# Performance work log

Measured on AMD Instinct MI355X. Metric: run time of the kernel, lower is better.

Reference implementation:

```python
import jax, jax.numpy as jnp
import numpy as np
from jax import lax

B, DIM, DIM_OUT, NH = 8, 512, 512, 8
HD = DIM_OUT // NH          # 64, also the depthwise-conv channel count
SQ, SKV = (1, 1), (2, 2)    # stride_q, stride_kv
PAD = 1                      # kernel 3 -> padding 3//2
SCALE = HD ** -0.5
EPS = 1e-6


def _dw_conv(x, w, stride):
    # x: [N, C, H, W], w: [C, 1, kh, kw]; depthwise conv (groups = C), no bias
    return lax.conv_general_dilated(
        x, w, window_strides=stride, padding=[(PAD, PAD), (PAD, PAD)],
        dimension_numbers=('NCHW', 'OIHW', 'NCHW'),
        feature_group_count=x.shape[1])


def _ln(x, w, b):
    m = jnp.mean(x, -1, keepdims=True)
    v = jnp.var(x, -1, keepdims=True)
    return (x - m) * lax.rsqrt(v + EPS) * w + b


def _pool(t, w, stride, ln_w, ln_b, H, W):
    # t: [B, NH, 1+H*W, HD] with cls token at index 0
    Bn = t.shape[0]
    cls = t[:, :, :1, :]
    body = t[:, :, 1:, :].reshape(Bn * NH, H, W, HD).transpose(0, 3, 1, 2)
    body = _dw_conv(body, w, stride)
    ph, pw = body.shape[2], body.shape[3]
    body = body.reshape(Bn, NH, HD, ph * pw).transpose(0, 1, 3, 2)
    out = jnp.concatenate([cls, body], axis=2)
    return _ln(out, ln_w, ln_b), (ph, pw)


def _rel_bias(r_q4, q_shape, k_shape, rel_pos_h, rel_pos_w):
    # r_q4: [B, NH, q_h*q_w, HD] (cls token stripped)
    q_h, q_w = q_shape
    k_h, k_w = k_shape

    def dist(qs, ks):
        qr, kr = max(ks / qs, 1.0), max(qs / ks, 1.0)
        d = np.arange(qs)[:, None] * qr - np.arange(ks)[None, :] * kr + (ks - 1) * kr
        return d.astype(np.int64)

    Rh = rel_pos_h[dist(q_h, k_h)]  # [q_h, k_h, HD]
    Rw = rel_pos_w[dist(q_w, k_w)]  # [q_w, k_w, HD]
    r_q = r_q4.reshape(r_q4.shape[0], NH, q_h, q_w, HD)
    rel_h = jnp.einsum('byhwc,hkc->byhwk', r_q, Rh)  # [B,NH,q_h,q_w,k_h]
    rel_w = jnp.einsum('byhwc,wkc->byhwk', r_q, Rw)  # [B,NH,q_h,q_w,k_w]
    return rel_h[..., :, None] + rel_w[..., None, :]  # [B,NH,q_h,q_w,k_h,k_w]


def setup_inputs() -> dict:
    key = jax.random.key(0)
    ks = jax.random.split(key, 16)
    H = W = 56
    N = H * W + 1
    rel_dim = 2 * H - 1  # 111
    return {
        'x': jax.random.normal(ks[0], (B, N, DIM), jnp.float32),
        'qkv_w': jax.random.normal(ks[1], (3 * DIM_OUT, DIM), jnp.float32) * DIM ** -0.5,
        'qkv_b': jax.random.normal(ks[2], (3 * DIM_OUT,), jnp.float32) * 0.02,
        'proj_w': jax.random.normal(ks[3], (DIM_OUT, DIM_OUT), jnp.float32) * DIM_OUT ** -0.5,
        'proj_b': jax.random.normal(ks[4], (DIM_OUT,), jnp.float32) * 0.02,
        'pool_q_w': jax.random.normal(ks[5], (HD, 1, 3, 3), jnp.float32) / 3.0,
        'pool_k_w': jax.random.normal(ks[6], (HD, 1, 3, 3), jnp.float32) / 3.0,
        'pool_v_w': jax.random.normal(ks[7], (HD, 1, 3, 3), jnp.float32) / 3.0,
        'lnq_w': 1.0 + 0.1 * jax.random.normal(ks[8], (HD,), jnp.float32),
        'lnq_b': 0.02 * jax.random.normal(ks[9], (HD,), jnp.float32),
        'lnk_w': 1.0 + 0.1 * jax.random.normal(ks[10], (HD,), jnp.float32),
        'lnk_b': 0.02 * jax.random.normal(ks[11], (HD,), jnp.float32),
        'lnv_w': 1.0 + 0.1 * jax.random.normal(ks[12], (HD,), jnp.float32),
        'lnv_b': 0.02 * jax.random.normal(ks[13], (HD,), jnp.float32),
        'rel_pos_h': 0.02 * jax.random.normal(ks[14], (rel_dim, HD), jnp.float32),
        'rel_pos_w': 0.02 * jax.random.normal(ks[15], (rel_dim, HD), jnp.float32),
        'hw_h': 56,
        'hw_w': 56,
    }


def reference(x, qkv_w, qkv_b, proj_w, proj_b, pool_q_w, pool_k_w, pool_v_w,
              lnq_w, lnq_b, lnk_w, lnk_b, lnv_w, lnv_b, rel_pos_h, rel_pos_w,
              hw_h, hw_w):
    Bn, N, _ = x.shape
    qkv = (x @ qkv_w.T + qkv_b).reshape(Bn, N, 3, NH, HD).transpose(2, 0, 3, 1, 4)
    q, k, v = qkv[0], qkv[1], qkv[2]  # each [B, NH, N, HD]
    q, q_shape = _pool(q, pool_q_w, SQ, lnq_w, lnq_b, hw_h, hw_w)
    k, k_shape = _pool(k, pool_k_w, SKV, lnk_w, lnk_b, hw_h, hw_w)
    v, _ = _pool(v, pool_v_w, SKV, lnv_w, lnv_b, hw_h, hw_w)
    attn = (q * SCALE) @ k.swapaxes(-2, -1)  # [B, NH, Nq, Nk]
    q_h, q_w = q_shape
    k_h, k_w = k_shape
    bias = _rel_bias(q[:, :, 1:, :], q_shape, k_shape, rel_pos_h, rel_pos_w)
    blk = attn[:, :, 1:, 1:].reshape(Bn, NH, q_h, q_w, k_h, k_w) + bias
    attn = attn.at[:, :, 1:, 1:].set(blk.reshape(Bn, NH, q_h * q_w, k_h * k_w))
    attn = jax.nn.softmax(attn, axis=-1)
    out = attn @ v                                   # [B, NH, Nq, HD]
    out = out.at[:, :, 1:, :].add(q[:, :, 1:, :])    # residual on non-cls rows
    out = out.transpose(0, 2, 1, 3).reshape(Bn, -1, DIM_OUT)
    return out @ proj_w.T + proj_b
```

## Files before the change

### kernel.cpp

```cpp
#include <hip/hip_runtime.h>
#include <hip/hip_bf16.h>
#include <cstdint>
#include <cstddef>

#define BB 8
#define NHH 8
#define NQ 3137
#define NKV 785
#define HDIM 64
#define AUG 128
#define MROWS (BB*NQ)
#define SCALE 0.125f
#define VTP 832

typedef unsigned short ushort_t;
typedef __attribute__((ext_vector_type(8))) short s16x8;
typedef __attribute__((ext_vector_type(4))) float f32x4;
typedef __attribute__((ext_vector_type(16))) float f32x16;

__device__ __forceinline__ float bf2f(ushort_t u) {
  union { unsigned int i; float f; } v; v.i = ((unsigned int)u) << 16; return v.f;
}
__device__ __forceinline__ ushort_t f2bf(float f) {
  union { float f; unsigned int i; } v; v.f = f;
  unsigned int r = v.i + 0x7fffu + ((v.i >> 16) & 1u);
  return (ushort_t)(r >> 16);
}
__device__ __forceinline__ unsigned int cvt_pk_bf16(float lo, float hi) {
  unsigned int r;
  asm("v_cvt_pk_bf16_f32 %0, %1, %2" : "=v"(r) : "v"(lo), "v"(hi));
  return r;
}
__device__ __forceinline__ s16x8 lds_frag8(const ushort_t* base, int row, int slot) {
  const char* p = (const char*)base + row * 128 + (((slot ^ (row & 7)) & 7) << 4);
  return *(const s16x8*)p;
}
__device__ __forceinline__ s16x8 lds_frag16(const ushort_t* base, int row, int slot) {
  const char* p = (const char*)base + row * 256 + (((slot ^ (row & 15)) & 15) << 4);
  return *(const s16x8*)p;
}

template<int EPI, bool AF32, bool WF32>
__global__ __launch_bounds__(256) void mfma_gemm_bt(
    const void* __restrict__ Ap, const void* __restrict__ Wp,
    const float* __restrict__ bias, void* __restrict__ outp, int M) {
  __shared__ ushort_t As[128][40];
  __shared__ ushort_t Bs[128][40];
  const int tid = threadIdx.x;
  const int l = tid & 63, w = tid >> 6;
  const int wr = w >> 1, wc = w & 1;
  const int lrow = l & 15, lk = l >> 4;
  const int m0 = blockIdx.y * 128, n0 = blockIdx.x * 128;
  const int srow = tid >> 2, sch = tid & 3;
  const int mA0 = m0 + srow      < M ? m0 + srow      : M - 1;
  const int mA1 = m0 + 64 + srow < M ? m0 + 64 + srow : M - 1;
  const size_t ar0 = (size_t)mA0 * 512, ar1 = (size_t)mA1 * 512;
  const size_t br0 = (size_t)(n0 + srow) * 512, br1 = (size_t)(n0 + 64 + srow) * 512;
  const ushort_t* Ab = (const ushort_t*)Ap;
  const float*    Af = (const float*)Ap;
  const ushort_t* Wb = (const ushort_t*)Wp;
  const float*    Wf = (const float*)Wp;
  auto ld8 = [&](const ushort_t* pb, const float* pf, size_t ofs, bool f32) -> uint4 {
    if (!f32) return *(const uint4*)(pb + ofs);
    const float4 v0 = *(const float4*)(pf + ofs);
    const float4 v1 = *(const float4*)(pf + ofs + 4);
    uint4 r;
    r.x = cvt_pk_bf16(v0.x, v0.y); r.y = cvt_pk_bf16(v0.z, v0.w);
    r.z = cvt_pk_bf16(v1.x, v1.y); r.w = cvt_pk_bf16(v1.z, v1.w);
    return r;
  };
  f32x4 acc[4][4];
  #pragma unroll
  for (int i = 0; i < 4; ++i) {
    #pragma unroll
    for (int j = 0; j < 4; ++j) acc[i][j] = (f32x4){0.f, 0.f, 0.f, 0.f};
  }
  for (int k0 = 0; k0 < 512; k0 += 32) {
    const uint4 a0 = ld8(Ab, Af, ar0 + k0 + sch * 8, AF32);
    const uint4 a1 = ld8(Ab, Af, ar1 + k0 + sch * 8, AF32);
    const uint4 b0 = ld8(Wb, Wf, br0 + k0 + sch * 8, WF32);
    const uint4 b1 = ld8(Wb, Wf, br1 + k0 + sch * 8, WF32);
    __syncthreads();
    *(uint4*)(&As[srow][sch * 8])      = a0;
    *(uint4*)(&As[64 + srow][sch * 8]) = a1;
    *(uint4*)(&Bs[srow][sch * 8])      = b0;
    *(uint4*)(&Bs[64 + srow][sch * 8]) = b1;
    __syncthreads();
    s16x8 af[4], bfr[4];
    #pragma unroll
    for (int mi = 0; mi < 4; ++mi)
      af[mi] = *(const s16x8*)(&As[wr * 64 + mi * 16 + lrow][lk * 8]);
    #pragma unroll
    for (int ni = 0; ni < 4; ++ni)
      bfr[ni] = *(const s16x8*)(&Bs[wc * 64 + ni * 16 + lrow][lk * 8]);
    #pragma unroll
    for (int mi = 0; mi < 4; ++mi) {
      #pragma unroll
      for (int ni = 0; ni < 4; ++ni)
        acc[mi][ni] = __builtin_amdgcn_mfma_f32_16x16x32_bf16(
            af[mi], bfr[ni], acc[mi][ni], 0, 0, 0);
    }
  }
  #pragma unroll
  for (int mi = 0; mi < 4; ++mi) {
    #pragma unroll
    for (int r = 0; r < 4; ++r) {
      const int m = m0 + wr * 64 + mi * 16 + 4 * lk + r;
      if (m >= M) continue;
      #pragma unroll
      for (int ni = 0; ni < 4; ++ni) {
        const int n = n0 + wc * 64 + ni * 16 + lrow;
        const float v = acc[mi][ni][r] + bias[n];
        if (EPI == 0) {
          const int which = n >> 9, y = (n >> 6) & 7, c = n & 63;
          const int b_ = m / NQ, tok = m - b_ * NQ;
          ((ushort_t*)outp)[((((size_t)which * BB + b_) * NHH + y) * NQ + tok) * HDIM + c] = f2bf(v);
        } else {
          ((float*)outp)[(size_t)m * 512 + n] = v;
        }
      }
    }
  }
}

template<int MODE>
__global__ __launch_bounds__(256) void pool_ln_kernel(
    const ushort_t* __restrict__ in, ushort_t* __restrict__ out0,
    ushort_t* __restrict__ out1,
    const float* __restrict__ cw, const float* __restrict__ lnw,
    const float* __restrict__ lnb, int stride, int OW, int R) {
  const int tid = threadIdx.x;
  const int c = tid & 63;
  const int rid = blockIdx.x * 4 + (tid >> 6);
  const int by = rid / R;
  const int n = rid - by * R;
  const ushort_t* ibase = in + (size_t)by * NQ * HDIM;
  float val;
  if (n == 0) {
    val = bf2f(ibase[c]);
  } else {
    const int p = n - 1;
    const int ho = p / OW, wo = p - ho * OW;
    float s = 0.f;
    #pragma unroll
    for (int dh = 0; dh < 3; ++dh) {
      const int hh = ho * stride + dh - 1;
      if (hh < 0 || hh >= 56) continue;
      #pragma unroll
      for (int dw = 0; dw < 3; ++dw) {
        const int ww = wo * stride + dw - 1;
        if (ww < 0 || ww >= 56) continue;
        s += cw[c * 9 + dh * 3 + dw] * bf2f(ibase[(size_t)(1 + hh * 56 + ww) * HDIM + c]);
      }
    }
    val = s;
  }
  float sum = val, sq = val * val;
  #pragma unroll
  for (int off = 32; off > 0; off >>= 1) {
    sum += __shfl_xor(sum, off);
    sq  += __shfl_xor(sq,  off);
  }
  const float mean = sum * (1.f / 64.f);
  const float var  = sq * (1.f / 64.f) - mean * mean;
  const float rs = rsqrtf(var + 1e-6f);
  const float lno = (val - mean) * rs * lnw[c] + lnb[c];
  if (MODE == 0) {
    out0[(size_t)rid * HDIM + c] = f2bf(lno);
  } else if (MODE == 1) {
    out0[(size_t)rid * HDIM + c] = f2bf(lno);
    out1[(size_t)rid * AUG + c] = f2bf(lno * SCALE);
    out1[(size_t)rid * AUG + 64 + c] = 0;
  } else {
    out0[(size_t)rid * AUG + c] = f2bf(lno);
    ushort_t aug = 0;
    if (n >= 1) {
      const int p = n - 1;
      const int kh = p / 28, kw = p - 28 * kh;
      if (c < 28) { if (c == kh) aug = 0x3F80; }
      else if (c < 56) { if (c - 28 == kw) aug = 0x3F80; }
    }
    out0[(size_t)rid * AUG + 64 + c] = aug;
  }
}

__global__ __launch_bounds__(256) void transpose_v_kernel(
    const ushort_t* __restrict__ vin, ushort_t* __restrict__ vtout) {
  __shared__ ushort_t T[64][65];
  const int tid = threadIdx.x;
  const int by = blockIdx.y;
  const int n0 = blockIdx.x * 64;
  #pragma unroll
  for (int half = 0; half < 2; ++half) {
    const int idx = tid + half * 256;
    const int r = idx >> 3, s = idx & 7;
    const int n = n0 + r;
    uint4 d = make_uint4(0u, 0u, 0u, 0u);
    if (n < NKV) d = *(const uint4*)(vin + ((size_t)by * NKV + n) * HDIM + s * 8);
    const ushort_t* dp = (const ushort_t*)&d;
    #pragma unroll
    for (int e = 0; e < 8; ++e) T[r][s * 8 + e] = dp[e];
  }
  __syncthreads();
  #pragma unroll
  for (int half = 0; half < 2; ++half) {
    const int idx = tid + half * 256;
    const int c = idx >> 3, g = idx & 7;
    ushort_t pk[8];
    #pragma unroll
    for (int e = 0; e < 8; ++e) pk[e] = T[g * 8 + e][c];
    *(uint4*)(vtout + ((size_t)by * 64 + c) * VTP + n0 + g * 8) = *(const uint4*)pk;
  }
}

__global__ __launch_bounds__(256) void relbias_mfma_kernel(
    const ushort_t* __restrict__ qb, const float* __restrict__ rph,
    const float* __restrict__ rpw, ushort_t* __restrict__ qaug) {
  const int tid = threadIdx.x;
  const int l = tid & 63, w = tid >> 6;
  const int lrow = l & 15, lk = l >> 4;
  const int hw = blockIdx.y;
  const int mode = blockIdx.z;
  const int r0 = blockIdx.x * 256 + w * 64;
  const float* tab = mode ? rpw : rph;
  s16x8 bfr[2][2];
  #pragma unroll
  for (int ni = 0; ni < 2; ++ni) {
    const int kh = ni * 16 + lrow;
    int trow = hw - 2 * kh + 54;
    if (trow < 0) trow = 0;
    const float* tr = tab + (size_t)trow * 64 + lk * 8;
    #pragma unroll
    for (int k0 = 0; k0 < 2; ++k0) {
      const float4 t0 = *(const float4*)(tr + k0 * 32);
      const float4 t1 = *(const float4*)(tr + k0 * 32 + 4);
      s16x8 bb;
      bb[0] = (short)f2bf(t0.x); bb[1] = (short)f2bf(t0.y);
      bb[2] = (short)f2bf(t0.z); bb[3] = (short)f2bf(t0.w);
      bb[4] = (short)f2bf(t1.x); bb[5] = (short)f2bf(t1.y);
      bb[6] = (short)f2bf(t1.z); bb[7] = (short)f2bf(t1.w);
      bfr[ni][k0] = bb;
    }
  }
  s16x8 af[4][2];
  #pragma unroll
  for (int mi = 0; mi < 4; ++mi) {
    const int rA = r0 + mi * 16 + lrow;
    const int by = rA / 56, oth = rA - 56 * by;
    const int tok = mode ? (1 + oth * 56 + hw) : (1 + hw * 56 + oth);
    const ushort_t* qp = qb + ((size_t)by * NQ + tok) * HDIM + lk * 8;
    af[mi][0] = *(const s16x8*)(qp);
    af[mi][1] = *(const s16x8*)(qp + 32);
  }
  f32x4 acc[4][2];
  #pragma unroll
  for (int mi = 0; mi < 4; ++mi) {
    #pragma unroll
    for (int ni = 0; ni < 2; ++ni) acc[mi][ni] = (f32x4){0.f, 0.f, 0.f, 0.f};
  }
  #pragma unroll
  for (int k0 = 0; k0 < 2; ++k0) {
    #pragma unroll
    for (int mi = 0; mi < 4; ++mi) {
      #pragma unroll
      for (int ni = 0; ni < 2; ++ni)
        acc[mi][ni] = __builtin_amdgcn_mfma_f32_16x16x32_bf16(
            af[mi][k0], bfr[ni][k0], acc[mi][ni], 0, 0, 0);
    }
  }
  const int augofs = 64 + mode * 28;
  #pragma unroll
  for (int mi = 0; mi < 4; ++mi) {
    #pragma unroll
    for (int r = 0; r < 4; ++r) {
      const int row = r0 + mi * 16 + 4 * lk + r;
      const int by = row / 56, oth = row - 56 * by;
      const int tok = 1 + (mode ? (oth * 56 + hw) : (hw * 56 + oth));
      ushort_t* orow = qaug + ((size_t)by * NQ + tok) * AUG + augofs;
      #pragma unroll
      for (int ni = 0; ni < 2; ++ni) {
        const int kh = ni * 16 + lrow;
        if (kh < 28) orow[kh] = f2bf(acc[mi][ni][r]);
      }
    }
  }
}

__global__ __launch_bounds__(256) void attn_mfma32_kernel(
    const ushort_t* __restrict__ qaug, const ushort_t* __restrict__ kaug,
    const ushort_t* __restrict__ qb, const ushort_t* __restrict__ vt,
    ushort_t* __restrict__ outp) {
  __shared__ ushort_t Kl[64 * AUG];
  __shared__ ushort_t Vl[64 * 64];
  const int tid = threadIdx.x;
  const int l = tid & 63;
  const int w = tid >> 6;
  const int h = l >> 5, q5 = l & 31;
  const int by = blockIdx.y;
  const int qt0 = blockIdx.x * 128;
  const int qloc = w * 32 + q5;
  const int qglob = qt0 + qloc;
  const int qcl = qglob < NQ ? qglob : NQ - 1;
  const ushort_t* qrow = qaug + ((size_t)by * NQ + qcl) * AUG;
  s16x8 qf[8];
  #pragma unroll
  for (int cb = 0; cb < 8; ++cb)
    qf[cb] = *(const s16x8*)(qrow + cb * 16 + h * 8);
  f32x16 ot0, ot1;
  #pragma unroll
  for (int i = 0; i < 16; ++i) { ot0[i] = 0.f; ot1[i] = 0.f; }
  float mr = -1e30f, lr = 0.f;
  const int krow = tid >> 2, ks4 = (tid & 3) * 4;
  const int vrow = tid >> 3, vslot = tid & 7;
  const ushort_t* kbase = kaug + (size_t)by * NKV * AUG + ks4 * 8;
  const ushort_t* vbase0 = vt + ((size_t)by * 64 + vrow) * VTP + vslot * 8;
  const ushort_t* vbase1 = vt + ((size_t)by * 64 + vrow + 32) * VTP + vslot * 8;
  uint4 kreg[4], vreg[2];
  auto load_tile = [&](int j0) {
    int jK = j0 + krow; if (jK > NKV - 1) jK = NKV - 1;
    const ushort_t* ksrc = kbase + (size_t)jK * AUG;
    kreg[0] = *(const uint4*)(ksrc);
    kreg[1] = *(const uint4*)(ksrc + 8);
    kreg[2] = *(const uint4*)(ksrc + 16);
    kreg[3] = *(const uint4*)(ksrc + 24);
    vreg[0] = *(const uint4*)(vbase0 + j0);
    vreg[1] = *(const uint4*)(vbase1 + j0);
  };
  auto store_tile = [&]() {
    char* kb_ = (char*)Kl + krow * 256;
    const int rm = krow & 15;
    *(uint4*)(kb_ + (((ks4 + 0) ^ rm) << 4)) = kreg[0];
    *(uint4*)(kb_ + (((ks4 + 1) ^ rm) << 4)) = kreg[1];
    *(uint4*)(kb_ + (((ks4 + 2) ^ rm) << 4)) = kreg[2];
    *(uint4*)(kb_ + (((ks4 + 3) ^ rm) << 4)) = kreg[3];
    *(uint4*)((char*)Vl + vrow * 128 + (((vslot ^ (vrow & 7)) & 7) << 4)) = vreg[0];
    *(uint4*)((char*)Vl + (vrow + 32) * 128 + (((vslot ^ ((vrow + 32) & 7)) & 7) << 4)) = vreg[1];
  };
  load_tile(0);
  #pragma unroll 1
  for (int it = 0; it < 13; ++it) {
    __syncthreads();
    store_tile();
    __syncthreads();
    if (it < 12) load_tile((it + 1) * 64);
    f32x16 st0, st1;
    #pragma unroll
    for (int i = 0; i < 16; ++i) { st0[i] = 0.f; st1[i] = 0.f; }
    __builtin_amdgcn_s_setprio(1);
    #pragma unroll
    for (int cb = 0; cb < 8; ++cb) {
      st0 = __builtin_amdgcn_mfma_f32_32x32x16_bf16(
          lds_frag16(Kl, q5, cb * 2 + h), qf[cb], st0, 0, 0, 0);
      st1 = __builtin_amdgcn_mfma_f32_32x32x16_bf16(
          lds_frag16(Kl, 32 + q5, cb * 2 + h), qf[cb], st1, 0, 0, 0);
    }
    __builtin_amdgcn_s_setprio(0);
    if (it == 12) {
      #pragma unroll
      for (int r = 0; r < 16; ++r) {
        const int klocal = (r & 3) + 8 * (r >> 2) + 4 * h;
        if (768 + klocal >= NKV) st0[r] = -1e30f;
        st1[r] = -1e30f;
      }
    }
    float mloc = st0[0];
    #pragma unroll
    for (int r = 1; r < 16; ++r) mloc = fmaxf(mloc, st0[r]);
    #pragma unroll
    for (int r = 0; r < 16; ++r) mloc = fmaxf(mloc, st1[r]);
    mloc = fmaxf(mloc, __shfl_xor(mloc, 32));
    if (!__all(mloc <= mr + 8.f)) {
      const float mn = fmaxf(mr, mloc);
      const float sc = __expf(mr - mn);
      mr = mn;
      lr *= sc;
      #pragma unroll
      for (int i = 0; i < 16; ++i) { ot0[i] *= sc; ot1[i] *= sc; }
    }
    float ps = 0.f;
    #pragma unroll
    for (int r = 0; r < 16; ++r) { st0[r] = __expf(st0[r] - mr); ps += st0[r]; }
    #pragma unroll
    for (int r = 0; r < 16; ++r) { st1[r] = __expf(st1[r] - mr); ps += st1[r]; }
    ps += __shfl_xor(ps, 32);
    lr += ps;
    auto pvstep = [&](const f32x16& pv, int kt) {
      #pragma unroll
      for (int kbk = 0; kbk < 2; ++kbk) {
        const unsigned int pk01 = cvt_pk_bf16(pv[kbk * 8 + 0], pv[kbk * 8 + 1]);
        const unsigned int pk23 = cvt_pk_bf16(pv[kbk * 8 + 2], pv[kbk * 8 + 3]);
        const unsigned int pk45 = cvt_pk_bf16(pv[kbk * 8 + 4], pv[kbk * 8 + 5]);
        const unsigned int pk67 = cvt_pk_bf16(pv[kbk * 8 + 6], pv[kbk * 8 + 7]);
        const unsigned int sA = (unsigned int)__shfl_xor((int)pk01, 32);
        const unsigned int sB = (unsigned int)__shfl_xor((int)pk45, 32);
        const unsigned int sC = (unsigned int)__shfl_xor((int)pk23, 32);
        const unsigned int sD = (unsigned int)__shfl_xor((int)pk67, 32);
        int4 fw;
        fw.x = (int)(h ? sB : pk01);
        fw.y = (int)(h ? sD : pk23);
        fw.z = (int)(h ? pk45 : sA);
        fw.w = (int)(h ? pk67 : sC);
        s16x8 pf;
        __builtin_memcpy(&pf, &fw, 16);
        const int slot = kt * 4 + kbk * 2 + h;
        __builtin_amdgcn_s_setprio(1);
        ot0 = __builtin_amdgcn_mfma_f32_32x32x16_bf16(
            lds_frag8(Vl, q5, slot), pf, ot0, 0, 0, 0);
        ot1 = __builtin_amdgcn_mfma_f32_32x32x16_bf16(
            lds_frag8(Vl, 32 + q5, slot), pf, ot1, 0, 0, 0);
        __builtin_amdgcn_s_setprio(0);
      }
    };
    pvstep(st0, 0);
    pvstep(st1, 1);
  }
  const float inv = 1.f / lr;
  if (qglob < NQ) {
    const int b_ = by >> 3, y_ = by & 7;
    ushort_t* obase = outp + ((size_t)b_ * NQ + qglob) * 512 + (size_t)y_ * 64;
    const ushort_t* rbase = qb + ((size_t)by * NQ + qglob) * HDIM;
    #pragma unroll
    for (int ch = 0; ch < 2; ++ch) {
      #pragma unroll
      for (int rg = 0; rg < 4; ++rg) {
        const int c0 = ch * 32 + 8 * rg + 4 * h;
        float vv[4];
        #pragma unroll
        for (int e = 0; e < 4; ++e)
          vv[e] = (ch ? ot1[rg * 4 + e] : ot0[rg * 4 + e]) * inv;
        if (qglob > 0) {
          #pragma unroll
          for (int e = 0; e < 4; ++e) vv[e] += bf2f(rbase[c0 + e]);
        }
        ushort_t pk[4] = { f2bf(vv[0]), f2bf(vv[1]), f2bf(vv[2]), f2bf(vv[3]) };
        *(uint2*)(obase + c0) = *(const uint2*)pk;
      }
    }
  }
}

extern "C" void kernel_launch(void* const* d_in, const int* in_sizes, int n_in,
                              void* d_out, int out_size, void* d_ws, size_t ws_size,
                              hipStream_t stream) {
  const float* x        = (const float*)d_in[0];
  const float* qkv_w    = (const float*)d_in[1];
  const float* qkv_b    = (const float*)d_in[2];
  const float* proj_w   = (const float*)d_in[3];
  const float* proj_b   = (const float*)d_in[4];
  const float* pool_q_w = (const float*)d_in[5];
  const float* pool_k_w = (const float*)d_in[6];
  const float* pool_v_w = (const float*)d_in[7];
  const float* lnq_w    = (const float*)d_in[8];
  const float* lnq_b    = (const float*)d_in[9];
  const float* lnk_w    = (const float*)d_in[10];
  const float* lnk_b    = (const float*)d_in[11];
  const float* lnv_w    = (const float*)d_in[12];
  const float* lnv_b    = (const float*)d_in[13];
  const float* rel_pos_h = (const float*)d_in[14];
  const float* rel_pos_w = (const float*)d_in[15];

  constexpr size_t E1 = (size_t)BB * NHH * NQ * HDIM;
  char* ws = (char*)d_ws;
  size_t off = 0;
  ushort_t* qkv_raw = (ushort_t*)(ws + off); off += 3 * E1 * 2;
  ushort_t* q_bf    = (ushort_t*)(ws + off); off += E1 * 2;
  ushort_t* qaug    = (ushort_t*)(ws + off); off += (size_t)BB * NHH * NQ * AUG * 2;
  ushort_t* kaug    = (ushort_t*)(ws + off); off += (size_t)BB * NHH * NKV * AUG * 2;
  ushort_t* v_bf    = (ushort_t*)(ws + off); off += (size_t)BB * NHH * NKV * HDIM * 2;
  ushort_t* v_t     = (ushort_t*)(ws + off); off += (size_t)64 * 64 * VTP * 2;
  ushort_t* attn_bf = qkv_raw;

  mfma_gemm_bt<0, true, true><<<dim3(12, 197), 256, 0, stream>>>(
      x, qkv_w, qkv_b, (void*)qkv_raw, MROWS);

  pool_ln_kernel<1><<<(64 * NQ) / 4,  256, 0, stream>>>(qkv_raw,          q_bf, qaug, pool_q_w, lnq_w, lnq_b, 1, 56, NQ);
  pool_ln_kernel<2><<<(64 * NKV) / 4, 256, 0, stream>>>(qkv_raw + E1,     kaug, nullptr, pool_k_w, lnk_w, lnk_b, 2, 28, NKV);
  pool_ln_kernel<0><<<(64 * NKV) / 4, 256, 0, stream>>>(qkv_raw + 2 * E1, v_bf, nullptr, pool_v_w, lnv_w, lnv_b, 2, 28, NKV);

  transpose_v_kernel<<<dim3(13, 64), 256, 0, stream>>>(v_bf, v_t);

  relbias_mfma_kernel<<<dim3(14, 56, 2), 256, 0, stream>>>(q_bf, rel_pos_h, rel_pos_w, qaug);

  attn_mfma32_kernel<<<dim3(25, 64), 256, 0, stream>>>(qaug, kaug, q_bf, v_t, attn_bf);

  mfma_gemm_bt<1, false, true><<<dim3(4, 197), 256, 0, stream>>>(
      attn_bf, proj_w, proj_b, d_out, MROWS);
}
```

Baseline: 556.0 us.

## Write K/V in MFMA fragment order and load attention operands directly from global

The pooling+LayerNorm kernels for K and V now write their outputs, padded to 800 rows, in a pre-swizzled MFMA-fragment layout, so each lane reads its 16-byte operand with one contiguous load. The attention kernel drops its LDS staging of K/V tiles and the two block barriers per iteration, and reads fragments straight from global/L2. The separate V-transpose kernel is removed. In exchange, every wave now fetches K/V from cache on its own, with no LDS sharing across the block's four waves, and no software prefetch hides that latency.

```diff
diff --git a/kernel.cpp b/kernel.cpp
--- a/kernel.cpp
+++ b/kernel.cpp
@@ -11,7 +11,7 @@
 #define AUG 128
 #define MROWS (BB*NQ)
 #define SCALE 0.125f
-#define VTP 832
+#define NKV_PAD 800
 
 typedef unsigned short ushort_t;
 typedef __attribute__((ext_vector_type(8))) short s16x8;
@@ -30,14 +30,6 @@
   unsigned int r;
   asm("v_cvt_pk_bf16_f32 %0, %1, %2" : "=v"(r) : "v"(lo), "v"(hi));
   return r;
-}
-__device__ __forceinline__ s16x8 lds_frag8(const ushort_t* base, int row, int slot) {
-  const char* p = (const char*)base + row * 128 + (((slot ^ (row & 7)) & 7) << 4);
-  return *(const s16x8*)p;
-}
-__device__ __forceinline__ s16x8 lds_frag16(const ushort_t* base, int row, int slot) {
-  const char* p = (const char*)base + row * 256 + (((slot ^ (row & 15)) & 15) << 4);
-  return *(const s16x8*)p;
 }
 
 template<int EPI, bool AF32, bool WF32>
@@ -128,32 +120,35 @@
     const ushort_t* __restrict__ in, ushort_t* __restrict__ out0,
     ushort_t* __restrict__ out1,
     const float* __restrict__ cw, const float* __restrict__ lnw,
-    const float* __restrict__ lnb, int stride, int OW, int R) {
+    const float* __restrict__ lnb, int stride, int OW, int R, int Rp) {
   const int tid = threadIdx.x;
   const int c = tid & 63;
   const int rid = blockIdx.x * 4 + (tid >> 6);
-  const int by = rid / R;
-  const int n = rid - by * R;
+  const int by = rid / Rp;
+  const int n = rid - by * Rp;
+  const bool vrow = (n < R);
   const ushort_t* ibase = in + (size_t)by * NQ * HDIM;
-  float val;
-  if (n == 0) {
-    val = bf2f(ibase[c]);
-  } else {
-    const int p = n - 1;
-    const int ho = p / OW, wo = p - ho * OW;
-    float s = 0.f;
-    #pragma unroll
-    for (int dh = 0; dh < 3; ++dh) {
-      const int hh = ho * stride + dh - 1;
-      if (hh < 0 || hh >= 56) continue;
-      #pragma unroll
-      for (int dw = 0; dw < 3; ++dw) {
-        const int ww = wo * stride + dw - 1;
-        if (ww < 0 || ww >= 56) continue;
-        s += cw[c * 9 + dh * 3 + dw] * bf2f(ibase[(size_t)(1 + hh * 56 + ww) * HDIM + c]);
-      }
-    }
-    val = s;
+  float val = 0.f;
+  if (vrow) {
+    if (n == 0) {
+      val = bf2f(ibase[c]);
+    } else {
+      const int p = n - 1;
+      const int ho = p / OW, wo = p - ho * OW;
+      float s = 0.f;
+      #pragma unroll
+      for (int dh = 0; dh < 3; ++dh) {
+        const int hh = ho * stride + dh - 1;
+        if (hh < 0 || hh >= 56) continue;
+        #pragma unroll
+        for (int dw = 0; dw < 3; ++dw) {
+          const int ww = wo * stride + dw - 1;
+          if (ww < 0 || ww >= 56) continue;
+          s += cw[c * 9 + dh * 3 + dw] * bf2f(ibase[(size_t)(1 + hh * 56 + ww) * HDIM + c]);
+        }
+      }
+      val = s;
+    }
   }
   float sum = val, sq = val * val;
   #pragma unroll
@@ -165,51 +160,36 @@
   const float var  = sq * (1.f / 64.f) - mean * mean;
   const float rs = rsqrtf(var + 1e-6f);
   const float lno = (val - mean) * rs * lnw[c] + lnb[c];
-  if (MODE == 0) {
-    out0[(size_t)rid * HDIM + c] = f2bf(lno);
-  } else if (MODE == 1) {
+  if (MODE == 1) {
     out0[(size_t)rid * HDIM + c] = f2bf(lno);
     out1[(size_t)rid * AUG + c] = f2bf(lno * SCALE);
     out1[(size_t)rid * AUG + 64 + c] = 0;
+  } else if (MODE == 2) {
+    const size_t base = ((size_t)by * 25 + (n >> 5)) * 8;
+    const int lf = n & 31;
+    {
+      const int ch = c;
+      const size_t ofs = (base + (ch >> 4)) * 512 +
+                         (size_t)(lf | (((ch >> 3) & 1) << 5)) * 8 + (ch & 7);
+      out0[ofs] = vrow ? f2bf(lno) : (ushort_t)0;
+    }
+    {
+      const int ch = 64 + c;
+      ushort_t aug = 0;
+      if (vrow && n >= 1) {
+        const int p = n - 1;
+        const int kh = p / 28, kw = p - 28 * kh;
+        if (c < 28) { if (c == kh) aug = 0x3F80; }
+        else if (c < 56) { if (c - 28 == kw) aug = 0x3F80; }
+      }
+      const size_t ofs = (base + (ch >> 4)) * 512 +
+                         (size_t)(lf | (((ch >> 3) & 1) << 5)) * 8 + (ch & 7);
+      out0[ofs] = aug;
+    }
   } else {
-    out0[(size_t)rid * AUG + c] = f2bf(lno);
-    ushort_t aug = 0;
-    if (n >= 1) {
-      const int p = n - 1;
-      const int kh = p / 28, kw = p - 28 * kh;
-      if (c < 28) { if (c == kh) aug = 0x3F80; }
-      else if (c < 56) { if (c - 28 == kw) aug = 0x3F80; }
-    }
-    out0[(size_t)rid * AUG + 64 + c] = aug;
-  }
-}
-
-__global__ __launch_bounds__(256) void transpose_v_kernel(
-    const ushort_t* __restrict__ vin, ushort_t* __restrict__ vtout) {
-  __shared__ ushort_t T[64][65];
-  const int tid = threadIdx.x;
-  const int by = blockIdx.y;
-  const int n0 = blockIdx.x * 64;
-  #pragma unroll
-  for (int half = 0; half < 2; ++half) {
-    const int idx = tid + half * 256;
-    const int r = idx >> 3, s = idx & 7;
-    const int n = n0 + r;
-    uint4 d = make_uint4(0u, 0u, 0u, 0u);
-    if (n < NKV) d = *(const uint4*)(vin + ((size_t)by * NKV + n) * HDIM + s * 8);
-    const ushort_t* dp = (const ushort_t*)&d;
-    #pragma unroll
-    for (int e = 0; e < 8; ++e) T[r][s * 8 + e] = dp[e];
-  }
-  __syncthreads();
-  #pragma unroll
-  for (int half = 0; half < 2; ++half) {
-    const int idx = tid + half * 256;
-    const int c = idx >> 3, g = idx & 7;
-    ushort_t pk[8];
-    #pragma unroll
-    for (int e = 0; e < 8; ++e) pk[e] = T[g * 8 + e][c];
-    *(uint4*)(vtout + ((size_t)by * 64 + c) * VTP + n0 + g * 8) = *(const uint4*)pk;
+    const size_t ofs = (((size_t)by * 50 + (n >> 4)) * 2 + (c >> 5)) * 512 +
+                       (size_t)((c & 31) | (((n >> 3) & 1) << 5)) * 8 + (n & 7);
+    out0[ofs] = vrow ? f2bf(lno) : (ushort_t)0;
   }
 }
 
@@ -287,11 +267,9 @@
 }
 
 __global__ __launch_bounds__(256) void attn_mfma32_kernel(
-    const ushort_t* __restrict__ qaug, const ushort_t* __restrict__ kaug,
-    const ushort_t* __restrict__ qb, const ushort_t* __restrict__ vt,
+    const ushort_t* __restrict__ qaug, const ushort_t* __restrict__ kfrag,
+    const ushort_t* __restrict__ vfrag, const ushort_t* __restrict__ qb,
     ushort_t* __restrict__ outp) {
-  __shared__ ushort_t Kl[64 * AUG];
-  __shared__ ushort_t Vl[64 * 64];
   const int tid = threadIdx.x;
   const int l = tid & 63;
   const int w = tid >> 6;
@@ -310,49 +288,22 @@
   #pragma unroll
   for (int i = 0; i < 16; ++i) { ot0[i] = 0.f; ot1[i] = 0.f; }
   float mr = -1e30f, lr = 0.f;
-  const int krow = tid >> 2, ks4 = (tid & 3) * 4;
-  const int vrow = tid >> 3, vslot = tid & 7;
-  const ushort_t* kbase = kaug + (size_t)by * NKV * AUG + ks4 * 8;
-  const ushort_t* vbase0 = vt + ((size_t)by * 64 + vrow) * VTP + vslot * 8;
-  const ushort_t* vbase1 = vt + ((size_t)by * 64 + vrow + 32) * VTP + vslot * 8;
-  uint4 kreg[4], vreg[2];
-  auto load_tile = [&](int j0) {
-    int jK = j0 + krow; if (jK > NKV - 1) jK = NKV - 1;
-    const ushort_t* ksrc = kbase + (size_t)jK * AUG;
-    kreg[0] = *(const uint4*)(ksrc);
-    kreg[1] = *(const uint4*)(ksrc + 8);
-    kreg[2] = *(const uint4*)(ksrc + 16);
-    kreg[3] = *(const uint4*)(ksrc + 24);
-    vreg[0] = *(const uint4*)(vbase0 + j0);
-    vreg[1] = *(const uint4*)(vbase1 + j0);
-  };
-  auto store_tile = [&]() {
-    char* kb_ = (char*)Kl + krow * 256;
-    const int rm = krow & 15;
-    *(uint4*)(kb_ + (((ks4 + 0) ^ rm) << 4)) = kreg[0];
-    *(uint4*)(kb_ + (((ks4 + 1) ^ rm) << 4)) = kreg[1];
-    *(uint4*)(kb_ + (((ks4 + 2) ^ rm) << 4)) = kreg[2];
-    *(uint4*)(kb_ + (((ks4 + 3) ^ rm) << 4)) = kreg[3];
-    *(uint4*)((char*)Vl + vrow * 128 + (((vslot ^ (vrow & 7)) & 7) << 4)) = vreg[0];
-    *(uint4*)((char*)Vl + (vrow + 32) * 128 + (((vslot ^ ((vrow + 32) & 7)) & 7) << 4)) = vreg[1];
-  };
-  load_tile(0);
+  const ushort_t* kfb = kfrag + (size_t)by * 25 * 8 * 512 + (size_t)l * 8;
+  const ushort_t* vfb = vfrag + (size_t)by * 50 * 2 * 512 + (size_t)l * 8;
   #pragma unroll 1
   for (int it = 0; it < 13; ++it) {
-    __syncthreads();
-    store_tile();
-    __syncthreads();
-    if (it < 12) load_tile((it + 1) * 64);
+    const int jt0 = 2 * it;
+    const int jt1 = (2 * it + 1 < 25) ? 2 * it + 1 : 24;
     f32x16 st0, st1;
     #pragma unroll
     for (int i = 0; i < 16; ++i) { st0[i] = 0.f; st1[i] = 0.f; }
     __builtin_amdgcn_s_setprio(1);
     #pragma unroll
     for (int cb = 0; cb < 8; ++cb) {
-      st0 = __builtin_amdgcn_mfma_f32_32x32x16_bf16(
-          lds_frag16(Kl, q5, cb * 2 + h), qf[cb], st0, 0, 0, 0);
-      st1 = __builtin_amdgcn_mfma_f32_32x32x16_bf16(
-          lds_frag16(Kl, 32 + q5, cb * 2 + h), qf[cb], st1, 0, 0, 0);
+      const s16x8 kf0 = *(const s16x8*)(kfb + (size_t)(jt0 * 8 + cb) * 512);
+      const s16x8 kf1 = *(const s16x8*)(kfb + (size_t)(jt1 * 8 + cb) * 512);
+      st0 = __builtin_amdgcn_mfma_f32_32x32x16_bf16(kf0, qf[cb], st0, 0, 0, 0);
+      st1 = __builtin_amdgcn_mfma_f32_32x32x16_bf16(kf1, qf[cb], st1, 0, 0, 0);
     }
     __builtin_amdgcn_s_setprio(0);
     if (it == 12) {
@@ -402,12 +353,13 @@
         fw.w = (int)(h ? pk67 : sC);
         s16x8 pf;
         __builtin_memcpy(&pf, &fw, 16);
-        const int slot = kt * 4 + kbk * 2 + h;
+        int g = it * 4 + kt * 2 + kbk;
+        if (g > 49) g = 49;
+        const s16x8 v0 = *(const s16x8*)(vfb + (size_t)(g * 2 + 0) * 512);
+        const s16x8 v1 = *(const s16x8*)(vfb + (size_t)(g * 2 + 1) * 512);
         __builtin_amdgcn_s_setprio(1);
-        ot0 = __builtin_amdgcn_mfma_f32_32x32x16_bf16(
-            lds_frag8(Vl, q5, slot), pf, ot0, 0, 0, 0);
-        ot1 = __builtin_amdgcn_mfma_f32_32x32x16_bf16(
-            lds_frag8(Vl, 32 + q5, slot), pf, ot1, 0, 0, 0);
+        ot0 = __builtin_amdgcn_mfma_f32_32x32x16_bf16(v0, pf, ot0, 0, 0, 0);
+        ot1 = __builtin_amdgcn_mfma_f32_32x32x16_bf16(v1, pf, ot1, 0, 0, 0);
         __builtin_amdgcn_s_setprio(0);
       }
     };
@@ -465,23 +417,23 @@
   ushort_t* qkv_raw = (ushort_t*)(ws + off); off += 3 * E1 * 2;
   ushort_t* q_bf    = (ushort_t*)(ws + off); off += E1 * 2;
   ushort_t* qaug    = (ushort_t*)(ws + off); off += (size_t)BB * NHH * NQ * AUG * 2;
-  ushort_t* kaug    = (ushort_t*)(ws + off); off += (size_t)BB * NHH * NKV * AUG * 2;
-  ushort_t* v_bf    = (ushort_t*)(ws + off); off += (size_t)BB * NHH * NKV * HDIM * 2;
-  ushort_t* v_t     = (ushort_t*)(ws + off); off += (size_t)64 * 64 * VTP * 2;
+  ushort_t* kfrag   = (ushort_t*)(ws + off); off += (size_t)64 * 25 * 8 * 512 * 2;
+  ushort_t* vfrag   = (ushort_t*)(ws + off); off += (size_t)64 * 50 * 2 * 512 * 2;
   ushort_t* attn_bf = qkv_raw;
 
   mfma_gemm_bt<0, true, true><<<dim3(12, 197), 256, 0, stream>>>(
       x, qkv_w, qkv_b, (void*)qkv_raw, MROWS);
 
-  pool_ln_kernel<1><<<(64 * NQ) / 4,  256, 0, stream>>>(qkv_raw,          q_bf, qaug, pool_q_w, lnq_w, lnq_b, 1, 56, NQ);
-  pool_ln_kernel<2><<<(64 * NKV) / 4, 256, 0, stream>>>(qkv_raw + E1,     kaug, nullptr, pool_k_w, lnk_w, lnk_b, 2, 28, NKV);
-  pool_ln_kernel<0><<<(64 * NKV) / 4, 256, 0, stream>>>(qkv_raw + 2 * E1, v_bf, nullptr, pool_v_w, lnv_w, lnv_b, 2, 28, NKV);
-
-  transpose_v_kernel<<<dim3(13, 64), 256, 0, stream>>>(v_bf, v_t);
+  pool_ln_kernel<1><<<(64 * NQ) / 4, 256, 0, stream>>>(
+      qkv_raw, q_bf, qaug, pool_q_w, lnq_w, lnq_b, 1, 56, NQ, NQ);
+  pool_ln_kernel<2><<<(64 * NKV_PAD) / 4, 256, 0, stream>>>(
+      qkv_raw + E1, kfrag, nullptr, pool_k_w, lnk_w, lnk_b, 2, 28, NKV, NKV_PAD);
+  pool_ln_kernel<0><<<(64 * NKV_PAD) / 4, 256, 0, stream>>>(
+      qkv_raw + 2 * E1, vfrag, nullptr, pool_v_w, lnv_w, lnv_b, 2, 28, NKV, NKV_PAD);
 
   relbias_mfma_kernel<<<dim3(14, 56, 2), 256, 0, stream>>>(q_bf, rel_pos_h, rel_pos_w, qaug);
 
-  attn_mfma32_kernel<<<dim3(25, 64), 256, 0, stream>>>(qaug, kaug, q_bf, v_t, attn_bf);
+  attn_mfma32_kernel<<<dim3(25, 64), 256, 0, stream>>>(qaug, kfrag, vfrag, q_bf, attn_bf);
 
   mfma_gemm_bt<1, false, true><<<dim3(4, 197), 256, 0, stream>>>(
       attn_bf, proj_w, proj_b, d_out, MROWS);
```

Measured after the change: 524.3 us. 1.06x faster.
